# Kernel optimization log

Measured on AMD Instinct MI355X. Metric: run time of the kernel, lower is better.

## Reference

```python
import jax, jax.numpy as jnp
import numpy as np

DIM = 1024
HEADS = 16
HEAD_DIM = DIM // HEADS
DFF = 4 * DIM  # SwiGLU expansion=4.0
EPS = 1e-5
NEG = -1e4  # original uses -1e4 causal mask, not -inf


def rms_norm(x, w):
    v = jnp.mean(x * x, axis=-1, keepdims=True)
    return w * (x * jax.lax.rsqrt(v + EPS))


def rotate_half(x):
    x1, x2 = jnp.split(x, 2, axis=-1)
    return jnp.concatenate((-x2, x1), axis=-1)


def setup_inputs() -> dict:
    key = jax.random.key(0)
    ks = jax.random.split(key, 12)
    B, S = 2, 2048
    s = 0.02
    h = jax.random.normal(ks[0], (B, S, DIM), jnp.float32)
    # RoPE tables, half-split convention: emb = concat(freqs, freqs)
    inv_freq = 1.0 / (10000.0 ** (np.arange(0, HEAD_DIM, 2, dtype=np.float32) / HEAD_DIM))
    freqs = np.arange(S, dtype=np.float32)[:, None] * inv_freq[None, :]
    emb = np.concatenate([freqs, freqs], axis=-1)
    cos = jnp.asarray(np.cos(emb))  # [S, HEAD_DIM]
    sin = jnp.asarray(np.sin(emb))
    return {
        "h": h, "cos": cos, "sin": sin,
        "norm1_w": jnp.ones((DIM,), jnp.float32),
        "wq": jax.random.normal(ks[1], (DIM, DIM), jnp.float32) * s,
        "wk": jax.random.normal(ks[2], (DIM, DIM), jnp.float32) * s,
        "wv": jax.random.normal(ks[3], (DIM, DIM), jnp.float32) * s,
        "wo": jax.random.normal(ks[4], (DIM, DIM), jnp.float32) * s,
        "norm2_w": jnp.ones((DIM,), jnp.float32),
        "gate_w": jax.random.normal(ks[5], (DFF, DIM), jnp.float32) * s,
        "gate_b": jnp.zeros((DFF,), jnp.float32),
        "up_w": jax.random.normal(ks[6], (DFF, DIM), jnp.float32) * s,
        "up_b": jnp.zeros((DFF,), jnp.float32),
        "down_w": jax.random.normal(ks[7], (DIM, DFF), jnp.float32) * s,
        "down_b": jnp.zeros((DIM,), jnp.float32),
        "gate": jnp.full((DIM,), 0.5, jnp.float32),
    }


def reference(h, cos, sin, norm1_w, wq, wk, wv, wo, norm2_w,
              gate_w, gate_b, up_w, up_b, down_w, down_b, gate):
    B, S, _ = h.shape
    scale = HEAD_DIM ** -0.5

    x = rms_norm(h, norm1_w)

    def heads(t):  # [B,S,DIM] -> [B,H,S,D]
        return t.reshape(B, S, HEADS, HEAD_DIM).transpose(0, 2, 1, 3)

    q = heads(x @ wq.T)
    k = heads(x @ wk.T)
    v = heads(x @ wv.T)

    # inline RoPE (cos/sin broadcast [S,D] over [B,H,S,D])
    q = q * cos + rotate_half(q) * sin
    k = k * cos + rotate_half(k) * sin

    scores = jnp.einsum('bhsd,bhtd->bhst', q, k) * scale
    causal = jnp.triu(jnp.full((S, S), NEG, jnp.float32), k=1)
    scores = scores + causal
    attn = jax.nn.softmax(scores, axis=-1)
    out = jnp.einsum('bhst,bhtd->bhsd', attn, v)
    out = out.transpose(0, 2, 1, 3).reshape(B, S, DIM)
    attn_out = out @ wo.T

    h = h + attn_out

    x2 = rms_norm(h, norm2_w)
    g = jax.nn.silu(x2 @ gate_w.T + gate_b)
    u = x2 @ up_w.T + up_b
    mlp = (g * u) @ down_w.T + down_b

    h = h + jax.nn.sigmoid(gate) * mlp
    return h
```

## Files before the change

### kernel.cpp

```cpp
#include <hip/hip_runtime.h>
#include <math.h>

#define DIM    1024
#define HEADS  16
#define HD     64
#define SEQ    2048
#define BATCH  2
#define TTOK   4096
#define DFF    4096
#define S3     3072
#define KSW    1024
#define NTSW   16

typedef __attribute__((ext_vector_type(8))) short short8;
typedef __attribute__((ext_vector_type(4))) float f32x4;

__device__ __forceinline__ float bf2f(unsigned short u) {
  union { unsigned int u; float f; } v; v.u = ((unsigned int)u) << 16; return v.f;
}
__device__ __forceinline__ unsigned short f2bf(float f) {
  union { float f; unsigned int u; } v; v.f = f;
  return (unsigned short)((v.u + 0x7FFFu + ((v.u >> 16) & 1u)) >> 16);
}
__device__ __forceinline__ unsigned short f2bf_trunc(float f) {
  union { float f; unsigned int u; } v; v.f = f;
  return (unsigned short)(v.u >> 16);
}

#define AS1(p) ((const __attribute__((address_space(1))) void*)(p))
#define AS3(p) ((__attribute__((address_space(3))) void*)(p))

__global__ __launch_bounds__(256) void wconv_k(
    const float* __restrict__ s0, const float* __restrict__ s1,
    const float* __restrict__ s2, const float* __restrict__ s3,
    const float* __restrict__ s4, const float* __restrict__ s5,
    const float* __restrict__ s6, unsigned short* __restrict__ dst)
{
  const int i = blockIdx.x * 256 + threadIdx.x;
  const float* s; int base; int di = i;
  if (i < 1048576) {
    if (i < 524288) { if (i < 262144) { s = s0; base = 0; } else { s = s1; base = 262144; } }
    else            { if (i < 786432) { s = s2; base = 524288; } else { s = s3; base = 786432; } }
  } else if (i < 2097152) {
    s = s4; base = 1048576;
    const int u = i - base; const int r = u >> 8; const int c = u & 255;
    di = 1048576 + (((r >> 4) << 5) + (r & 15)) * 256 + c;
  } else if (i < 3145728) {
    s = s5; base = 2097152;
    const int u = i - base; const int r = u >> 8; const int c = u & 255;
    di = 1048576 + (((r >> 4) << 5) + 16 + (r & 15)) * 256 + c;
  } else {
    s = s6; base = 3145728;
  }
  const float4 f = ((const float4*)s)[i - base];
  unsigned long long o = (unsigned long long)f2bf(f.x)
                       | ((unsigned long long)f2bf(f.y) << 16)
                       | ((unsigned long long)f2bf(f.z) << 32)
                       | ((unsigned long long)f2bf(f.w) << 48);
  ((unsigned long long*)dst)[di] = o;
}

template<int MODE>
__global__ __launch_bounds__(256) void gemm_bt(
    const unsigned short* __restrict__ A,
    const unsigned short* __restrict__ W,
    unsigned short* __restrict__ C,
    float* __restrict__ Cf,
    const float* __restrict__ resf,
    const float* __restrict__ cosp,
    const float* __restrict__ sinp,
    int M, int N, int K)
{
  __shared__ __align__(16) unsigned short As[128 * 64];
  __shared__ __align__(16) unsigned short Bs[128 * 64];

  const int tid  = threadIdx.x;
  const int lane = tid & 63;
  const int wv   = tid >> 6;
  const int row0 = blockIdx.x * 128;
  const int col0 = blockIdx.y * 128;
  const int wm   = (wv >> 1) * 64;
  const int wn   = (wv & 1) * 64;
  const int lr   = lane & 15;
  const int lg   = lane >> 4;

  const int srow = lane >> 3;
  const int skg  = (lane & 7) ^ srow;

  int kb = 0, ke = K;
  if (MODE == 6) { kb = blockIdx.z * 1024; ke = kb + 1024; }

  f32x4 acc[4][4];
#pragma unroll
  for (int i = 0; i < 4; i++)
#pragma unroll
    for (int j = 0; j < 4; j++) acc[i][j] = (f32x4){0.f, 0.f, 0.f, 0.f};

  for (int k0 = kb; k0 < ke; k0 += 64) {
#pragma unroll
    for (int i = 0; i < 4; i++) {
      const int c = wv * 4 + i;
      const unsigned short* ga = A + (size_t)(row0 + c * 8 + srow) * K + k0 + skg * 8;
      __builtin_amdgcn_global_load_lds(AS1(ga), AS3(As + c * 512), 16, 0, 0);
      const unsigned short* gb = W + (size_t)(col0 + c * 8 + srow) * K + k0 + skg * 8;
      __builtin_amdgcn_global_load_lds(AS1(gb), AS3(Bs + c * 512), 16, 0, 0);
    }
    __syncthreads();

#pragma unroll
    for (int ks = 0; ks < 2; ks++) {
      short8 af[4], bf[4];
#pragma unroll
      for (int i = 0; i < 4; i++) {
        const int r = wm + i * 16 + lr;
        af[i] = *(const short8*)(As + r * 64 + (((ks * 4 + lg) ^ (lr & 7)) * 8));
      }
#pragma unroll
      for (int j = 0; j < 4; j++) {
        const int r = wn + j * 16 + lr;
        bf[j] = *(const short8*)(Bs + r * 64 + (((ks * 4 + lg) ^ (lr & 7)) * 8));
      }
#pragma unroll
      for (int i = 0; i < 4; i++)
#pragma unroll
        for (int j = 0; j < 4; j++)
          acc[i][j] = __builtin_amdgcn_mfma_f32_16x16x32_bf16(af[i], bf[j], acc[i][j], 0, 0, 0);
    }
    __syncthreads();
  }

  if (MODE == 5) {
    const bool do_rope = (col0 < 2048);
#pragma unroll
    for (int i = 0; i < 4; i++) {
#pragma unroll
      for (int r = 0; r < 4; r++) {
        const int row = row0 + wm + i * 16 + lg * 4 + r;
        const int s = row & (SEQ - 1);
        const size_t rb = (size_t)row * N + col0 + wn;
        if (do_rope) {
#pragma unroll
          for (int jp = 0; jp < 2; jp++) {
            const int d = jp * 16 + lr;
            const float c = cosp[s * HD + d];
            const float sn = sinp[s * HD + d];
            const float x1v = acc[i][jp][r];
            const float x2v = acc[i][jp + 2][r];
            C[rb + d]      = f2bf(x1v * c - x2v * sn);
            C[rb + d + 32] = f2bf(x2v * c + x1v * sn);
          }
        } else {
#pragma unroll
          for (int j = 0; j < 4; j++)
            C[rb + j * 16 + lr] = f2bf(acc[i][j][r]);
        }
      }
    }
    return;
  }

  unsigned short* Cz = C;
  if (MODE == 6) {
    const size_t pz[4] = {4u * 1048576u, 8u * 1048576u, 16u * 1048576u, 0u};
    Cz = C + pz[blockIdx.z];
  }
#pragma unroll
  for (int i = 0; i < 4; i++) {
#pragma unroll
    for (int j = 0; j < 4; j++) {
      const int col = col0 + wn + j * 16 + lr;
#pragma unroll
      for (int r = 0; r < 4; r++) {
        const int row = row0 + wm + i * 16 + lg * 4 + r;
        const float v = acc[i][j][r];
        const size_t idx = (size_t)row * N + col;
        if (MODE == 3) {
          Cf[idx] = v + resf[idx];
        } else if (MODE == 6) {
          Cz[idx] = f2bf(v);
        }
      }
    }
  }
}

__global__ __launch_bounds__(512, 2) void gemm256_swiglu(
    const unsigned short* __restrict__ A,
    const unsigned short* __restrict__ W,
    unsigned short* __restrict__ G,
    const float* __restrict__ gbias,
    const float* __restrict__ ubias)
{
  __shared__ __align__(16) unsigned short Asl[2 * 16384];
  __shared__ __align__(16) unsigned short Bsl[2 * 16384];

  const int tid  = threadIdx.x;
  const int lane = tid & 63;
  const int wv   = tid >> 6;
  const int row0 = blockIdx.x * 256;
  const int col0 = blockIdx.y * 256;
  const int wm   = (wv >> 2) * 128;
  const int wn   = (wv & 3) * 64;
  const int lr   = lane & 15;
  const int lg   = lane >> 4;

  const int rl   = tid >> 3;
  const int rq   = (rl & 31) + ((rl >> 5) << 7);
  const int cl8  = ((tid & 7) ^ (rl & 7)) * 8;
  const int ldsu = wv * 512;

  auto stA = [&](int t, int q) {
    const unsigned short* s = A + (size_t)(row0 + q * 32 + rq) * KSW + t * 64 + cl8;
    __builtin_amdgcn_global_load_lds(AS1(s), AS3(Asl + (t & 1) * 16384 + q * 4096 + ldsu), 16, 0, 0);
  };
  auto stB = [&](int t, int q) {
    const unsigned short* s = W + (size_t)(col0 + q * 32 + rq) * KSW + t * 64 + cl8;
    __builtin_amdgcn_global_load_lds(AS1(s), AS3(Bsl + (t & 1) * 16384 + q * 4096 + ldsu), 16, 0, 0);
  };

  f32x4 acc[8][4];
#pragma unroll
  for (int f = 0; f < 8; f++)
#pragma unroll
    for (int j = 0; j < 4; j++) acc[f][j] = (f32x4){0.f, 0.f, 0.f, 0.f};

  stB(0, 0); stB(0, 1); stB(0, 2); stB(0, 3);
  stA(0, 0); stA(0, 1); stA(0, 2); stA(0, 3);
  stB(1, 0); stB(1, 1); stB(1, 2); stB(1, 3);
  stA(1, 0); stA(1, 1);
  asm volatile("s_waitcnt vmcnt(6)" ::: "memory");
  __builtin_amdgcn_s_barrier();

#pragma unroll 1
  for (int J = 0; J < NTSW / 2; ++J) {
    const int t2 = 2 * J + 2, t3 = 2 * J + 3;
#pragma unroll
    for (int h = 0; h < 2; ++h) {
      const unsigned short* Ab = Asl + h * 16384;
      const unsigned short* Bb = Bsl + h * 16384;
      short8 bfr[4][2];
#pragma unroll
      for (int p = 0; p < 4; ++p) {
        if (p == 0) {
#pragma unroll
          for (int j = 0; j < 4; ++j) {
            const int rn   = wn + j * 16 + lr;
            const int q    = (rn & 127) >> 5;
            const int rloc = (rn & 31) + ((rn >> 7) << 5);
#pragma unroll
            for (int ks = 0; ks < 2; ++ks)
              bfr[j][ks] = *(const short8*)(Bb + q * 4096 + rloc * 64 +
                                            (((ks * 4 + lg) ^ (lr & 7)) * 8));
          }
        }
        short8 af[2][2];
#pragma unroll
        for (int e = 0; e < 2; ++e) {
          const int rloc = e * 16 + lr + ((wv >> 2) << 5);
#pragma unroll
          for (int ks = 0; ks < 2; ++ks)
            af[e][ks] = *(const short8*)(Ab + p * 4096 + rloc * 64 +
                                         (((ks * 4 + lg) ^ (lr & 7)) * 8));
        }
        if (h == 0) {
          if (p == 0)      { stA(2 * J + 1, 2); stA(2 * J + 1, 3); }
          else if (p == 1) { if (t2 < NTSW) { stB(t2, 0); stB(t2, 1); } }
          else if (p == 2) { if (t2 < NTSW) { stB(t2, 2); stB(t2, 3); } }
          else {
            if (t2 < NTSW) { stA(t2, 0); stA(t2, 1);
                             asm volatile("s_waitcnt vmcnt(6)" ::: "memory"); }
            else           { asm volatile("s_waitcnt vmcnt(0)" ::: "memory"); }
          }
        } else {
          if (p == 0)      { if (t2 < NTSW) { stA(t2, 2); stA(t2, 3); } }
          else if (p == 1) { if (t3 < NTSW) { stB(t3, 0); stB(t3, 1); } }
          else if (p == 2) { if (t3 < NTSW) { stB(t3, 2); stB(t3, 3); } }
          else {
            if (t3 < NTSW) { stA(t3, 0); stA(t3, 1);
                             asm volatile("s_waitcnt vmcnt(6)" ::: "memory"); }
            else           { asm volatile("s_waitcnt vmcnt(0)" ::: "memory"); }
          }
        }
        __builtin_amdgcn_s_barrier();
        asm volatile("s_waitcnt lgkmcnt(0)" ::: "memory");
        __builtin_amdgcn_sched_barrier(0);
        __builtin_amdgcn_s_setprio(1);
#pragma unroll
        for (int e = 0; e < 2; ++e)
#pragma unroll
          for (int j = 0; j < 4; ++j)
#pragma unroll
            for (int ks = 0; ks < 2; ++ks)
              acc[2 * p + e][j] = __builtin_amdgcn_mfma_f32_16x16x32_bf16(
                  af[e][ks], bfr[j][ks], acc[2 * p + e][j], 0, 0, 0);
        __builtin_amdgcn_s_setprio(0);
        __builtin_amdgcn_s_barrier();
      }
    }
  }

  const int cb = (col0 + wn) >> 1;
#pragma unroll
  for (int jp = 0; jp < 2; ++jp) {
    const int lcol = cb + jp * 16 + lr;
    const float gbv = gbias[lcol];
    const float ubv = ubias[lcol];
#pragma unroll
    for (int f = 0; f < 8; ++f) {
#pragma unroll
      for (int r = 0; r < 4; ++r) {
        const int row = row0 + wm + f * 16 + lg * 4 + r;
        float gv = acc[f][2 * jp][r] + gbv;
        gv = gv / (1.0f + __expf(-gv));
        const float uv = acc[f][2 * jp + 1][r] + ubv;
        G[(size_t)row * DFF + lcol] = f2bf(gv * uv);
      }
    }
  }
}

__global__ __launch_bounds__(256) void dcomb_k(
    const unsigned short* __restrict__ ws, float* __restrict__ out,
    const float* __restrict__ db, const float* __restrict__ gate)
{
  const int i4 = blockIdx.x * 256 + threadIdx.x;
  const size_t idx = (size_t)i4 * 4;
  const int col = (int)(idx & 1023);
  const unsigned long long p0 = *(const unsigned long long*)(ws + 4u * 1048576u + idx);
  const unsigned long long p1 = *(const unsigned long long*)(ws + 8u * 1048576u + idx);
  const unsigned long long p2 = *(const unsigned long long*)(ws + 16u * 1048576u + idx);
  const unsigned long long p3 = *(const unsigned long long*)(ws + idx);
  float4 o = *(float4*)(out + idx);
  float* op = (float*)&o;
#pragma unroll
  for (int w = 0; w < 4; w++) {
    const float s = bf2f((unsigned short)(p0 >> (16 * w)))
                  + bf2f((unsigned short)(p1 >> (16 * w)))
                  + bf2f((unsigned short)(p2 >> (16 * w)))
                  + bf2f((unsigned short)(p3 >> (16 * w)))
                  + db[col + w];
    const float sg = 1.0f / (1.0f + __expf(-gate[col + w]));
    op[w] += sg * s;
  }
  *(float4*)(out + idx) = o;
}

template<int XF32>
__global__ __launch_bounds__(256) void rmsnorm_k(
    const void* __restrict__ Xv,
    const float* __restrict__ W,
    unsigned short* __restrict__ Y)
{
  const int t  = blockIdx.x;
  const int i0 = threadIdx.x * 4;

  float v[4];
  if (XF32) {
    const float4 f = *(const float4*)((const float*)Xv + (size_t)t * DIM + i0);
    v[0] = f.x; v[1] = f.y; v[2] = f.z; v[3] = f.w;
  } else {
    unsigned long long raw = *(const unsigned long long*)((const unsigned short*)Xv + (size_t)t * DIM + i0);
#pragma unroll
    for (int k = 0; k < 4; k++) v[k] = bf2f((unsigned short)(raw >> (16 * k)));
  }

  float ss = v[0] * v[0] + v[1] * v[1] + v[2] * v[2] + v[3] * v[3];
#pragma unroll
  for (int off = 32; off > 0; off >>= 1) ss += __shfl_xor(ss, off);

  __shared__ float red[4];
  if ((threadIdx.x & 63) == 0) red[threadIdx.x >> 6] = ss;
  __syncthreads();
  const float tot = red[0] + red[1] + red[2] + red[3];
  const float r = rsqrtf(tot * (1.0f / DIM) + 1e-5f);

  const float4 wf = *(const float4*)(W + i0);
  const float wv4[4] = {wf.x, wf.y, wf.z, wf.w};
  unsigned long long o = 0;
#pragma unroll
  for (int k = 0; k < 4; k++)
    o |= ((unsigned long long)f2bf(v[k] * r * wv4[k])) << (16 * k);
  *(unsigned long long*)(Y + (size_t)t * DIM + i0) = o;
}

__device__ const unsigned char cqt[32] = {10,10,15,15,9,9,13,14,14,14,15,4,8,8,12,12,13,13,7,7,11,11,11,12,3,6,6,5,5,2,1,0};
__device__ const unsigned char ctb[32] = {0,11,0,11,0,10,0,0,10,20,22,0,0,9,0,9,10,19,0,8,0,8,16,18,0,0,7,0,6,0,0,0};
__device__ const unsigned char ccnt[32] = {11,11,11,11,10,10,10,10,10,10,10,10,9,9,9,9,9,9,8,8,8,8,8,8,8,7,7,6,6,6,4,2};
__device__ const unsigned char cchv[32] = {0,1,0,1,0,1,0,0,1,2,2,0,0,1,0,1,1,2,0,1,0,1,2,2,0,0,1,0,1,0,0,0};
__device__ const unsigned char cpsv[32] = {255,5,255,14,255,4,255,255,12,13,15,255,255,3,255,8,10,11,255,2,255,6,7,9,255,255,1,255,0,255,255,255};

__global__ __launch_bounds__(256) void fattn_k(
    const unsigned short* __restrict__ QKV,
    unsigned short* __restrict__ O,
    unsigned short* __restrict__ Pbuf,
    float* __restrict__ Lbuf)
{
  __shared__ __align__(16) unsigned short Ks[2][64 * 64];
  __shared__ __align__(16) unsigned short Vt[2][64 * 72];
  __shared__ __align__(16) unsigned short Ps[4 * 32 * 72];

  const int tid  = threadIdx.x;
  const int lane = tid & 63;
  const int wv   = tid >> 6;
  const int lr   = lane & 15;
  const int lg   = lane >> 4;

  const int j  = blockIdx.x;
  const int bh = blockIdx.y;
  const int qt = cqt[j];
  const int tb = ctb[j];
  const int nt = ccnt[j];
  const int ch = cchv[j];
  const int ps = cpsv[j];
  const int b  = bh >> 4, h = bh & 15;
  const int q0 = qt * 128;
  const size_t rowb = (size_t)b * SEQ;
  const int qoff = h * HD;
  const int koff = 1024 + qoff;
  const int voff = 2048 + qoff;

  short8 aq[2][2];
#pragma unroll
  for (int rf = 0; rf < 2; rf++) {
    const size_t tok = rowb + q0 + wv * 32 + rf * 16 + lr;
    aq[rf][0] = *(const short8*)(QKV + tok * S3 + qoff + lg * 8);
    aq[rf][1] = *(const short8*)(QKV + tok * S3 + qoff + 32 + lg * 8);
  }

  f32x4 o[2][4];
  f32x4 lacc[2];
#pragma unroll
  for (int rf = 0; rf < 2; rf++) {
    lacc[rf] = (f32x4){0.f, 0.f, 0.f, 0.f};
#pragma unroll
    for (int d = 0; d < 4; d++) o[rf][d] = (f32x4){0.f, 0.f, 0.f, 0.f};
  }
  short8 onesb;
#pragma unroll
  for (int jj = 0; jj < 8; jj++) onesb[jj] = (short)0x3F80;

  const int srow = lane >> 3;
  const int skg  = (lane & 7) ^ srow;
  const int kv   = tid >> 2;
  const int d0   = (tid & 3) * 16;

  const float C1 = 0.125f * 1.44269504f;
  const float C2 = 11.5415603f;

  auto stage = [&](int buf, int ti) {
    const int t0 = (tb + ti) * 64;
    unsigned short* ksb = &Ks[buf][0];
#pragma unroll
    for (int i = 0; i < 2; i++) {
      const int c = wv * 2 + i;
      const unsigned short* gk = QKV + (rowb + t0 + c * 8 + srow) * S3 + koff + skg * 8;
      __builtin_amdgcn_global_load_lds(AS1(gk), AS3(ksb + c * 512), 16, 0, 0);
    }
    unsigned short* vtb = &Vt[buf][0];
    const unsigned short* gv = QKV + (rowb + t0 + kv) * S3 + voff + d0;
    const short8 v0 = *(const short8*)gv;
    const short8 v1 = *(const short8*)(gv + 8);
    const int klo = kv & 7, khi = kv >> 3;
#pragma unroll
    for (int w = 0; w < 8; w++) {
      const int da = d0 + w, db2 = d0 + 8 + w;
      vtb[da  * 72 + ((khi ^ ((da  >> 3) & 7)) * 8) + klo] = (unsigned short)v0[w];
      vtb[db2 * 72 + ((khi ^ ((db2 >> 3) & 7)) * 8) + klo] = (unsigned short)v1[w];
    }
  };

  stage(0, 0);

  for (int ti = 0; ti < nt; ti++) {
    __syncthreads();
    if (ti + 1 < nt) stage((ti + 1) & 1, ti + 1);

    const int t0 = (tb + ti) * 64;
    const unsigned short* ksb = &Ks[ti & 1][0];
    const unsigned short* vtb = &Vt[ti & 1][0];

    f32x4 S[2][4];
#pragma unroll
    for (int sub = 0; sub < 4; sub++) {
      const int kr = sub * 16 + lr;
      const short8 bk0 = *(const short8*)(ksb + kr * 64 + ((lg       ^ (kr & 7)) * 8));
      const short8 bk1 = *(const short8*)(ksb + kr * 64 + (((4 + lg) ^ (kr & 7)) * 8));
#pragma unroll
      for (int rf = 0; rf < 2; rf++) {
        f32x4 s = (f32x4){0.f, 0.f, 0.f, 0.f};
        s = __builtin_amdgcn_mfma_f32_16x16x32_bf16(aq[rf][0], bk0, s, 0, 0, 0);
        s = __builtin_amdgcn_mfma_f32_16x16x32_bf16(aq[rf][1], bk1, s, 0, 0, 0);
        S[rf][sub] = s;
      }
    }

    unsigned short* pw = Ps + wv * (32 * 72);
#pragma unroll
    for (int rf = 0; rf < 2; rf++) {
      const int qmin = q0 + wv * 32 + rf * 16;
      const bool diag = (t0 + 63 > qmin);
#pragma unroll
      for (int sub = 0; sub < 4; sub++) {
#pragma unroll
        for (int r = 0; r < 4; r++) {
          float t = fmaf(S[rf][sub][r], C1, -C2);
          if (diag && (t0 + sub * 16 + lr > qmin + lg * 4 + r)) t = -INFINITY;
          const float p = exp2f(t);
          pw[(rf * 16 + lg * 4 + r) * 72 + sub * 16 + lr] = f2bf_trunc(p);
        }
      }
    }

#pragma unroll
    for (int kf = 0; kf < 2; kf++) {
      const short8 pa0 = *(const short8*)(pw + lr * 72 + kf * 32 + lg * 8);
      const short8 pa1 = *(const short8*)(pw + (16 + lr) * 72 + kf * 32 + lg * 8);
      lacc[0] = __builtin_amdgcn_mfma_f32_16x16x32_bf16(pa0, onesb, lacc[0], 0, 0, 0);
      lacc[1] = __builtin_amdgcn_mfma_f32_16x16x32_bf16(pa1, onesb, lacc[1], 0, 0, 0);
#pragma unroll
      for (int dsub = 0; dsub < 4; dsub++) {
        const int d = dsub * 16 + lr;
        const short8 bvf = *(const short8*)(vtb + d * 72 +
                             (((kf * 4 + lg) ^ ((d >> 3) & 7)) * 8));
        o[0][dsub] = __builtin_amdgcn_mfma_f32_16x16x32_bf16(pa0, bvf, o[0][dsub], 0, 0, 0);
        o[1][dsub] = __builtin_amdgcn_mfma_f32_16x16x32_bf16(pa1, bvf, o[1][dsub], 0, 0, 0);
      }
    }
  }

  if (ps == 255 && qt < 5) {
#pragma unroll
    for (int rf = 0; rf < 2; rf++) {
      float inv[4];
#pragma unroll
      for (int r = 0; r < 4; r++) inv[r] = 1.0f / lacc[rf][r];
#pragma unroll
      for (int dsub = 0; dsub < 4; dsub++)
#pragma unroll
        for (int r = 0; r < 4; r++)
          O[(rowb + q0 + wv * 32 + rf * 16 + lg * 4 + r) * DIM + h * HD + dsub * 16 + lr] =
              f2bf(o[rf][dsub][r] * inv[r]);
    }
  } else {
    const int lbase = ((bh * 11 + (qt - 5)) * 3 + ch) * 128;
#pragma unroll
    for (int rf = 0; rf < 2; rf++) {
      const int rbase = wv * 32 + rf * 16 + lg * 4;
      if (lr == 0) {
#pragma unroll
        for (int r = 0; r < 4; r++) Lbuf[lbase + rbase + r] = lacc[rf][r];
      }
    }
    if (ps == 255) {
#pragma unroll
      for (int rf = 0; rf < 2; rf++)
#pragma unroll
        for (int dsub = 0; dsub < 4; dsub++)
#pragma unroll
          for (int r = 0; r < 4; r++)
            O[(rowb + q0 + wv * 32 + rf * 16 + lg * 4 + r) * DIM + h * HD + dsub * 16 + lr] =
                f2bf(o[rf][dsub][r]);
    } else {
      unsigned short* pb = Pbuf + ((size_t)bh * 16 + ps) * 8192;
#pragma unroll
      for (int rf = 0; rf < 2; rf++) {
        const int rbase = wv * 32 + rf * 16 + lg * 4;
#pragma unroll
        for (int dsub = 0; dsub < 4; dsub++)
#pragma unroll
          for (int r = 0; r < 4; r++)
            pb[(rbase + r) * 64 + dsub * 16 + lr] = f2bf(o[rf][dsub][r]);
      }
    }
  }
}

__global__ __launch_bounds__(256) void fattn_combine_k(
    const unsigned short* __restrict__ Pbuf,
    const float* __restrict__ Lbuf,
    unsigned short* __restrict__ O)
{
  const int qt = 5 + blockIdx.x;
  const int bh = blockIdx.y;
  const int b  = bh >> 4, h = bh & 15;
  const int q0 = qt * 128;
  const size_t rowb = (size_t)b * SEQ;
  const int pbase_t[11] = {0, 1, 2, 3, 4, 5, 6, 8, 10, 12, 14};
  const int pb0 = pbase_t[qt - 5];
  const int np  = (qt < 11) ? 1 : 2;
  const int lbase = (bh * 11 + (qt - 5)) * 3 * 128;

  const unsigned short* p0 = Pbuf + ((size_t)bh * 16 + pb0) * 8192;
  const unsigned short* p1 = Pbuf + ((size_t)bh * 16 + pb0 + 1) * 8192;

#pragma unroll
  for (int it = 0; it < 4; it++) {
    const int idx = it * 2048 + threadIdx.x * 8;
    const int row = idx >> 6;
    const int col = idx & 63;
    float ls = Lbuf[lbase + row] + Lbuf[lbase + 128 + row];
    if (np == 2) ls += Lbuf[lbase + 256 + row];
    const float inv = 1.0f / ls;

    unsigned short* op = O + (rowb + q0 + row) * DIM + h * HD + col;
    const short8 vb = *(const short8*)op;
    const short8 e0 = *(const short8*)(p0 + idx);
    short8 e1;
    if (np == 2) e1 = *(const short8*)(p1 + idx);
    short8 r;
#pragma unroll
    for (int w = 0; w < 8; w++) {
      float s = bf2f((unsigned short)vb[w]) + bf2f((unsigned short)e0[w]);
      if (np == 2) s += bf2f((unsigned short)e1[w]);
      r[w] = (short)f2bf(s * inv);
    }
    *(short8*)op = r;
  }
}

extern "C" void kernel_launch(void* const* d_in, const int* in_sizes, int n_in,
                              void* d_out, int out_size, void* d_ws, size_t ws_size,
                              hipStream_t stream)
{
  const float* h    = (const float*)d_in[0];
  const float* cosb = (const float*)d_in[1];
  const float* sinb = (const float*)d_in[2];
  const float* n1w  = (const float*)d_in[3];
  const float* n2w  = (const float*)d_in[8];
  const float* gb   = (const float*)d_in[10];
  const float* ub   = (const float*)d_in[12];
  const float* db   = (const float*)d_in[14];
  const float* gatep= (const float*)d_in[15];
  float* out = (float*)d_out;

  unsigned short* ws = (unsigned short*)d_ws;
  const size_t M1 = 1u << 20;

  unsigned short* wqkv = ws;
  unsigned short* wo_c = ws + 3 * M1;
  unsigned short* gu_c = ws + 4 * M1;
  unsigned short* dw_c = ws + 12 * M1;
  unsigned short* x1   = ws + 16 * M1;
  unsigned short* Pbuf = ws + 16 * M1;
  unsigned short* x2   = ws + 16 * M1;
  float*          Lbuf = (float*)ws;
  unsigned short* qkv  = ws + 20 * M1;
  unsigned short* attn = ws + 32 * M1;
  unsigned short* g    = qkv;

  const dim3 blk(256);
  const dim3 gq(TTOK / 128, S3 / 128);
  const dim3 g1(TTOK / 128, DIM / 128);
  const dim3 gsw(TTOK / 256, (2 * DFF) / 256);
  const dim3 gd(TTOK / 128, DIM / 128, 4);

  wconv_k<<<16384, blk, 0, stream>>>(
      (const float*)d_in[4], (const float*)d_in[5], (const float*)d_in[6],
      (const float*)d_in[7], (const float*)d_in[9], (const float*)d_in[11],
      (const float*)d_in[13], ws);

  rmsnorm_k<1><<<TTOK, blk, 0, stream>>>(h, n1w, x1);

  gemm_bt<5><<<gq, blk, 0, stream>>>(x1, wqkv, qkv, nullptr, nullptr,
                                     cosb, sinb, TTOK, S3, DIM);

  fattn_k<<<dim3(32, BATCH * HEADS), blk, 0, stream>>>(qkv, attn, Pbuf, Lbuf);
  fattn_combine_k<<<dim3(11, BATCH * HEADS), blk, 0, stream>>>(Pbuf, Lbuf, attn);

  gemm_bt<3><<<g1, blk, 0, stream>>>(attn, wo_c, nullptr, out, h,
                                     nullptr, nullptr, TTOK, DIM, DIM);

  rmsnorm_k<1><<<TTOK, blk, 0, stream>>>(out, n2w, x2);

  gemm256_swiglu<<<gsw, dim3(512), 0, stream>>>(x2, gu_c, g, gb, ub);

  gemm_bt<6><<<gd, blk, 0, stream>>>(g, dw_c, ws, nullptr, nullptr,
                                     nullptr, nullptr, TTOK, DIM, DFF);

  dcomb_k<<<4096, blk, 0, stream>>>(ws, out, db, gatep);
}
```

Baseline: 426.9 us.

## Run split-K down projection on the 256x256 pipelined GEMM kernel

Templates the 256x256 double-buffered SwiGLU GEMM kernel so it can also do the split-K down projection, with a K offset per z-slice and a plain bf16 partial-output epilogue. The down-proj GEMM moves from the 128x128 single-buffered kernel to this kernel, with the grid shrunk to 16x4x4. The aim is higher operand reuse and better load/compute overlap. The cost is fewer blocks (256), which may leave CUs under-filled or give tail effects.

```diff
diff --git a/kernel.cpp b/kernel.cpp
--- a/kernel.cpp
+++ b/kernel.cpp
@@ -9,7 +9,6 @@
 #define TTOK   4096
 #define DFF    4096
 #define S3     3072
-#define KSW    1024
 #define NTSW   16
 
 typedef __attribute__((ext_vector_type(8))) short short8;
@@ -87,16 +86,13 @@
   const int srow = lane >> 3;
   const int skg  = (lane & 7) ^ srow;
 
-  int kb = 0, ke = K;
-  if (MODE == 6) { kb = blockIdx.z * 1024; ke = kb + 1024; }
-
   f32x4 acc[4][4];
 #pragma unroll
   for (int i = 0; i < 4; i++)
 #pragma unroll
     for (int j = 0; j < 4; j++) acc[i][j] = (f32x4){0.f, 0.f, 0.f, 0.f};
 
-  for (int k0 = kb; k0 < ke; k0 += 64) {
+  for (int k0 = 0; k0 < K; k0 += 64) {
 #pragma unroll
     for (int i = 0; i < 4; i++) {
       const int c = wv * 4 + i;
@@ -159,11 +155,6 @@
     return;
   }
 
-  unsigned short* Cz = C;
-  if (MODE == 6) {
-    const size_t pz[4] = {4u * 1048576u, 8u * 1048576u, 16u * 1048576u, 0u};
-    Cz = C + pz[blockIdx.z];
-  }
 #pragma unroll
   for (int i = 0; i < 4; i++) {
 #pragma unroll
@@ -176,20 +167,20 @@
         const size_t idx = (size_t)row * N + col;
         if (MODE == 3) {
           Cf[idx] = v + resf[idx];
-        } else if (MODE == 6) {
-          Cz[idx] = f2bf(v);
-        }
-      }
-    }
-  }
-}
-
-__global__ __launch_bounds__(512, 2) void gemm256_swiglu(
+        }
+      }
+    }
+  }
+}
+
+template<int MODE>
+__global__ __launch_bounds__(512, 2) void gemm256_k(
     const unsigned short* __restrict__ A,
     const unsigned short* __restrict__ W,
     unsigned short* __restrict__ G,
     const float* __restrict__ gbias,
-    const float* __restrict__ ubias)
+    const float* __restrict__ ubias,
+    int Kst)
 {
   __shared__ __align__(16) unsigned short Asl[2 * 16384];
   __shared__ __align__(16) unsigned short Bsl[2 * 16384];
@@ -203,6 +194,7 @@
   const int wn   = (wv & 3) * 64;
   const int lr   = lane & 15;
   const int lg   = lane >> 4;
+  const int kb   = (MODE == 6) ? blockIdx.z * 1024 : 0;
 
   const int rl   = tid >> 3;
   const int rq   = (rl & 31) + ((rl >> 5) << 7);
@@ -210,11 +202,11 @@
   const int ldsu = wv * 512;
 
   auto stA = [&](int t, int q) {
-    const unsigned short* s = A + (size_t)(row0 + q * 32 + rq) * KSW + t * 64 + cl8;
+    const unsigned short* s = A + (size_t)(row0 + q * 32 + rq) * Kst + kb + t * 64 + cl8;
     __builtin_amdgcn_global_load_lds(AS1(s), AS3(Asl + (t & 1) * 16384 + q * 4096 + ldsu), 16, 0, 0);
   };
   auto stB = [&](int t, int q) {
-    const unsigned short* s = W + (size_t)(col0 + q * 32 + rq) * KSW + t * 64 + cl8;
+    const unsigned short* s = W + (size_t)(col0 + q * 32 + rq) * Kst + kb + t * 64 + cl8;
     __builtin_amdgcn_global_load_lds(AS1(s), AS3(Bsl + (t & 1) * 16384 + q * 4096 + ldsu), 16, 0, 0);
   };
 
@@ -299,21 +291,38 @@
     }
   }
 
-  const int cb = (col0 + wn) >> 1;
-#pragma unroll
-  for (int jp = 0; jp < 2; ++jp) {
-    const int lcol = cb + jp * 16 + lr;
-    const float gbv = gbias[lcol];
-    const float ubv = ubias[lcol];
-#pragma unroll
-    for (int f = 0; f < 8; ++f) {
-#pragma unroll
-      for (int r = 0; r < 4; ++r) {
-        const int row = row0 + wm + f * 16 + lg * 4 + r;
-        float gv = acc[f][2 * jp][r] + gbv;
-        gv = gv / (1.0f + __expf(-gv));
-        const float uv = acc[f][2 * jp + 1][r] + ubv;
-        G[(size_t)row * DFF + lcol] = f2bf(gv * uv);
+  if (MODE == 7) {
+    const int cb = (col0 + wn) >> 1;
+#pragma unroll
+    for (int jp = 0; jp < 2; ++jp) {
+      const int lcol = cb + jp * 16 + lr;
+      const float gbv = gbias[lcol];
+      const float ubv = ubias[lcol];
+#pragma unroll
+      for (int f = 0; f < 8; ++f) {
+#pragma unroll
+        for (int r = 0; r < 4; ++r) {
+          const int row = row0 + wm + f * 16 + lg * 4 + r;
+          float gv = acc[f][2 * jp][r] + gbv;
+          gv = gv / (1.0f + __expf(-gv));
+          const float uv = acc[f][2 * jp + 1][r] + ubv;
+          G[(size_t)row * DFF + lcol] = f2bf(gv * uv);
+        }
+      }
+    }
+  } else {
+    const size_t pz[4] = {4u * 1048576u, 8u * 1048576u, 16u * 1048576u, 0u};
+    unsigned short* Cz = G + pz[blockIdx.z];
+#pragma unroll
+    for (int j = 0; j < 4; ++j) {
+      const int col = col0 + wn + j * 16 + lr;
+#pragma unroll
+      for (int f = 0; f < 8; ++f) {
+#pragma unroll
+        for (int r = 0; r < 4; ++r) {
+          const int row = row0 + wm + f * 16 + lg * 4 + r;
+          Cz[(size_t)row * DIM + col] = f2bf(acc[f][j][r]);
+        }
       }
     }
   }
@@ -652,7 +661,7 @@
   const dim3 gq(TTOK / 128, S3 / 128);
   const dim3 g1(TTOK / 128, DIM / 128);
   const dim3 gsw(TTOK / 256, (2 * DFF) / 256);
-  const dim3 gd(TTOK / 128, DIM / 128, 4);
+  const dim3 gd(TTOK / 256, DIM / 256, 4);
 
   wconv_k<<<16384, blk, 0, stream>>>(
       (const float*)d_in[4], (const float*)d_in[5], (const float*)d_in[6],
@@ -672,10 +681,9 @@
 
   rmsnorm_k<1><<<TTOK, blk, 0, stream>>>(out, n2w, x2);
 
-  gemm256_swiglu<<<gsw, dim3(512), 0, stream>>>(x2, gu_c, g, gb, ub);
-
-  gemm_bt<6><<<gd, blk, 0, stream>>>(g, dw_c, ws, nullptr, nullptr,
-                                     nullptr, nullptr, TTOK, DIM, DFF);
+  gemm256_k<7><<<gsw, dim3(512), 0, stream>>>(x2, gu_c, g, gb, ub, 1024);
+
+  gemm256_k<6><<<gd, dim3(512), 0, stream>>>(g, dw_c, ws, nullptr, nullptr, 4096);
 
   dcomb_k<<<4096, blk, 0, stream>>>(ws, out, db, gatep);
 }
```

After: 430.6 us. Within noise of the previous version (+0.9%).
